# Optimization experiments

Hardware: AMD Instinct MI355X
Metric: run time of the kernel (lower is better)

The kernel has to match this reference:

```python
import jax, jax.numpy as jnp
from jax import lax
import numpy as np

GAMMA, WARP = 0.01, 134.4          # SoftDTW(gamma=0.01, warp=134.4)
INF, BIG = 100000.0, 1e9           # INF from kl_loss_sdtw; BIG ~ math.inf boundary
KL_A, KL_FWD_A, GEN_A, GEN_E2E_A, FEAT_A, DUR_A, MEL_A = 1.0, 1.0, 1.0, 1.0, 1.0, 1.0, 45.0


def soft_dtw(D):
    """Soft-DTW with warp penalty. D: [B, N, M] -> R[:, N, M].
    R[i,j] = D[i-1,j-1] + softmin_gamma(R[i-1,j-1], R[i-1,j]+warp, R[i,j-1]+warp)."""
    B, N, M = D.shape
    row0 = jnp.full((B, M + 1), BIG, D.dtype).at[:, 0].set(0.0)  # R[0, :]

    def row_step(prev_row, d_row):                 # prev_row: [B, M+1], d_row: [B, M]
        left0 = jnp.full((B,), BIG, D.dtype)       # R[i, 0]

        def col_step(r_left, inp):
            d, r_diag, r_up = inp                  # each [B]
            r0 = -r_diag / GAMMA
            r1 = -(r_up + WARP) / GAMMA
            r2 = -(r_left + WARP) / GAMMA
            rmax = jnp.maximum(jnp.maximum(r0, r1), r2)
            smin = -GAMMA * (jnp.log(jnp.exp(r0 - rmax) + jnp.exp(r1 - rmax) + jnp.exp(r2 - rmax)) + rmax)
            r = d + smin
            return r, r

        xs = (d_row.T, prev_row[:, :-1].T, prev_row[:, 1:].T)   # scan over j=1..M
        _, vals = lax.scan(col_step, left0, xs)                 # [M, B]
        new_row = jnp.concatenate([left0[:, None], vals.T], axis=1)
        return new_row, None

    last, _ = lax.scan(row_step, row0, jnp.swapaxes(D, 0, 1))   # scan over i=1..N
    return last[:, M]


def sdtw_kl_matrix(z, logs_q, m, logs_p):
    """kl[b,i,j] = sum_h logs_p - logs_q - 0.5 + 0.5*(z-m)^2*exp(-2 logs_p).
    m, logs_p: [b,h,tp]; z, logs_q: [b,h,tq] -> [b,tp,tq] via 3 batched GEMMs."""
    h = m.shape[1]
    w = jnp.exp(-2.0 * logs_p)                                   # [b,h,tp]
    quad = (jnp.einsum('bhi,bhj->bij', w, z * z)
            - 2.0 * jnp.einsum('bhi,bhj->bij', w * m, z)
            + jnp.sum(w * m * m, axis=1)[:, :, None])
    return (jnp.sum(logs_p, axis=1)[:, :, None]
            - jnp.sum(logs_q, axis=1)[:, None, :]
            - 0.5 * h + 0.5 * quad)


def kl_loss_sdtw(z, logs_q, m, logs_p, p_mask, q_mask):
    kl = sdtw_kl_matrix(z, logs_q, m, logs_p)
    kl = jnp.pad(kl, ((0, 0), (0, 1), (0, 1)))
    pm = jnp.pad(p_mask, ((0, 0), (0, 1)))
    qm = jnp.pad(q_mask, ((0, 0), (0, 1)))
    pb = pm[:, :, None].astype(bool)
    qb = qm[:, None, :].astype(bool)
    kl = jnp.where(pb ^ qb, INF, kl)
    kl = jnp.where((~pb) & (~qb), 0.0, kl)
    return jnp.sum(soft_dtw(kl)) / jnp.sum(pm)


def _forward(mel_slice, mel_slice_hat, scores_disc_fake, scores_disc_fake_e2e,
             feats_disc_real, feats_disc_fake, loss_duration, loss_duration_len,
             loss_pitch, z_p, m_p, logs_p, z_q, m_q, logs_q, p_mask, z_mask):
    # generator losses: sum over discriminators of mean((1-score)^2)
    loss_gen = jnp.sum(jnp.mean((1.0 - scores_disc_fake) ** 2, axis=(1, 2))) * GEN_A
    loss_gen_e2e = jnp.sum(jnp.mean((1.0 - scores_disc_fake_e2e) ** 2, axis=(1, 2))) * GEN_E2E_A
    # feature-matching loss (real feats detached)
    fr = lax.stop_gradient(feats_disc_real)
    loss_fm = jnp.sum(jnp.mean(jnp.abs(fr - feats_disc_fake), axis=(1, 2, 3))) * 2.0 * FEAT_A
    loss_mel = jnp.mean(jnp.abs(mel_slice - mel_slice_hat)) * MEL_A
    loss_dur = jnp.sum(loss_duration) * DUR_A
    loss_dur_len = jnp.log(loss_duration_len + 1e-6)
    zm = z_mask[:, 0, :]
    loss_kl = kl_loss_sdtw(z_p, logs_q, m_p, logs_p, p_mask, zm) * KL_A
    loss_kl_fwd = kl_loss_sdtw(z_q, logs_p, m_q, logs_q, zm, p_mask) * KL_FWD_A
    return (loss_gen + loss_gen_e2e + loss_fm + loss_mel + loss_dur
            + loss_dur_len + loss_kl + loss_kl_fwd)


def setup_inputs() -> dict:
    key = jax.random.key(0)
    ks = jax.random.split(key, 16)
    B, H, TP, TQ = 4, 192, 350, 400
    return {
        'mel_slice': jax.random.normal(ks[0], (B, 80, 128), jnp.float32),
        'mel_slice_hat': jax.random.normal(ks[1], (B, 80, 128), jnp.float32),
        'scores_disc_fake': jax.random.normal(ks[2], (6, B, 8192), jnp.float32),
        'scores_disc_fake_e2e': jax.random.normal(ks[3], (6, B, 8192), jnp.float32),
        'feats_disc_real': jax.random.normal(ks[4], (24, B, 128, 4096), jnp.float32),
        'feats_disc_fake': jax.random.normal(ks[5], (24, B, 128, 4096), jnp.float32),
        'loss_duration': jax.random.uniform(ks[6], (B, TP), jnp.float32) * 0.01,
        'loss_duration_len': jax.random.uniform(ks[7], (), jnp.float32) + 0.5,
        'loss_pitch': jax.random.uniform(ks[8], (B, TP), jnp.float32),
        'z_p': jax.random.normal(ks[9], (B, H, TQ), jnp.float32),
        'm_p': jax.random.normal(ks[10], (B, H, TP), jnp.float32),
        'logs_p': 0.1 * jax.random.normal(ks[11], (B, H, TP), jnp.float32),
        'z_q': jax.random.normal(ks[12], (B, H, TP), jnp.float32),
        'm_q': jax.random.normal(ks[13], (B, H, TQ), jnp.float32),
        'logs_q': 0.1 * jax.random.normal(ks[14], (B, H, TQ), jnp.float32),
        'p_mask': jnp.ones((B, TP), jnp.float32),
        'z_mask': jnp.ones((B, 1, TQ), jnp.float32),
    }


def reference(mel_slice, mel_slice_hat, scores_disc_fake, scores_disc_fake_e2e,
              feats_disc_real, feats_disc_fake, loss_duration, loss_duration_len,
              loss_pitch, z_p, m_p, logs_p, z_q, m_q, logs_q, p_mask, z_mask):
    return _forward(mel_slice, mel_slice_hat, scores_disc_fake, scores_disc_fake_e2e,
                    feats_disc_real, feats_disc_fake, loss_duration, loss_duration_len,
                    loss_pitch, z_p, m_p, logs_p, z_q, m_q, logs_q, p_mask, z_mask)
```

## Files before the change

kernel.cpp:

```cpp
#include <hip/hip_runtime.h>
#include <math.h>

#define GAMMA_ 0.01f
#define WARP_  134.4f
#define INFV   100000.0f
#define BIGV   1000000000.0f

#define B_  4
#define H_  192
#define TP_ 350
#define TQ_ 400

#define ACC_OFF 0
#define DTW_OFF 16
#define SLP_OFF 32
#define SLQ_OFF (SLP_OFF + B_*TP_)
#define KL1_OFF 3072
#define KL1_NCOL 401
#define KL1_PITCHT 352
#define KL2_OFF (KL1_OFF + B_*KL1_NCOL*KL1_PITCHT)
#define KL2_NCOL 351
#define KL2_PITCHT 408

#define RING_SLOTS 67
#define RING_PITCH 416

typedef float f4_t __attribute__((ext_vector_type(4)));

__device__ __forceinline__ unsigned pk2(float a, float b) {
    unsigned ua = __float_as_uint(a), ub = __float_as_uint(b);
    ua = (ua + 0x7FFFu + ((ua >> 16) & 1u)) >> 16;
    ub = (ub + 0x7FFFu + ((ub >> 16) & 1u)) & 0xFFFF0000u;
    return ua | ub;
}
__device__ __forceinline__ int modS(int x) { return x - (x / RING_SLOTS) * RING_SLOTS; }

__global__ void sl_kernel(const float* __restrict__ logs_p,
                          const float* __restrict__ logs_q,
                          float* __restrict__ ws) {
    int t = blockIdx.x * 256 + threadIdx.x;
    if (t < 32) ws[ACC_OFF + t] = 0.f;
    if (t < B_ * TP_) {
        int b = t / TP_, i = t % TP_;
        const float* p = logs_p + (size_t)b * H_ * TP_ + i;
        float s = 0.f;
        for (int h = 0; h < H_; ++h) s += p[(size_t)h * TP_];
        ws[SLP_OFF + t] = s;
    } else if (t < B_ * TP_ + B_ * TQ_) {
        int t2 = t - B_ * TP_;
        int b = t2 / TQ_, j = t2 % TQ_;
        const float* p = logs_q + (size_t)b * H_ * TQ_ + j;
        float s = 0.f;
        for (int h = 0; h < H_; ++h) s += p[(size_t)h * TQ_];
        ws[SLQ_OFF + t2] = s;
    }
}

__global__ void kl_kernel(const float* __restrict__ mp, const float* __restrict__ lsp,
                          const float* __restrict__ zp,
                          const float* __restrict__ mq, const float* __restrict__ lsq,
                          const float* __restrict__ zq,
                          const float* __restrict__ pmask, const float* __restrict__ zmask,
                          float* __restrict__ ws) {
    int which = blockIdx.z >> 2;
    int b     = blockIdx.z & 3;
    const float *mS, *lS, *zS, *SLrow, *SLcol, *rm, *cm; float* out; int R, C, pitchT;
    if (which == 0) { mS=mp; lS=lsp; zS=zp; SLrow=ws+SLP_OFF; SLcol=ws+SLQ_OFF;
                      rm=pmask + b*TP_; cm=zmask + b*TQ_;
                      out=ws+KL1_OFF + (size_t)b*KL1_NCOL*KL1_PITCHT;
                      R=TP_; C=TQ_; pitchT=KL1_PITCHT; }
    else            { mS=mq; lS=lsq; zS=zq; SLrow=ws+SLQ_OFF; SLcol=ws+SLP_OFF;
                      rm=zmask + b*TQ_; cm=pmask + b*TP_;
                      out=ws+KL2_OFF + (size_t)b*KL2_NCOL*KL2_PITCHT;
                      R=TQ_; C=TP_; pitchT=KL2_PITCHT; }
// ... 23 lines not shown
            zSh[hh][cc] = (gj < C) ? zB[(size_t)h * C + gj] : 0.f;
        }
        __syncthreads();
#pragma unroll
        for (int kk = 0; kk < 16; ++kk) {
            float2 wv = *(const float2*)&wS [kk][tx * 2];
            float2 mv = *(const float2*)&mSh[kk][tx * 2];
            float2 zv = *(const float2*)&zSh[kk][ty * 2];
            float d;
            d = zv.x - mv.x; a00 += wv.x * d * d;
            d = zv.x - mv.y; a01 += wv.y * d * d;
            d = zv.y - mv.x; a10 += wv.x * d * d;
            d = zv.y - mv.y; a11 += wv.y * d * d;
        }
        __syncthreads();
    }
    float accs[2][2] = {{a00, a01}, {a10, a11}};
    for (int jj = 0; jj < 2; ++jj)
        for (int ii = 0; ii < 2; ++ii) {
            int I = i0 + tx * 2 + ii, J = j0 + ty * 2 + jj;
            if (I <= R && J <= C) {
                bool pbI = (I < R) && (rm[I] != 0.f);
                bool qbJ = (J < C) && (cm[J] != 0.f);
                float v;
                if (pbI & qbJ)
                    v = SLrow[b * R + I] - SLcol[b * C + J] - 0.5f * H_ + 0.5f * accs[jj][ii];
                else
                    v = (pbI ^ qbJ) ? INFV : 0.f;
                out[(size_t)J * pitchT + I] = v;
            }
        }
}

#define SLD2(BK, q) { int col_; \
    col_ = ((q) << 3) + cA; \
    if (vA && col_ <= C_) rA##BK = *(const f4_t*)(klT + (size_t)col_ * pitchT + (iA << 2)); \
    col_ = ((q) << 3) + cB; \
    if (vB && col_ <= C_) rB##BK = *(const f4_t*)(klT + (size_t)col_ * pitchT + (iB << 2)); }
#define SST2(BK, q) { int col_; \
    col_ = ((q) << 3) + cA; \
    if (vA && col_ <= C_) { int s_ = modS(col_); \
        uint2 u_; u_.x = pk2(rA##BK.x, rA##BK.y); u_.y = pk2(rA##BK.z, rA##BK.w); \
        *(uint2*)&ring[s_][iA << 2] = u_; } \
    col_ = ((q) << 3) + cB; \
    if (vB && col_ <= C_) { int s_ = modS(col_); \
        uint2 u_; u_.x = pk2(rB##BK.x, rB##BK.y); u_.y = pk2(rB##BK.z, rB##BK.w); \
        *(uint2*)&ring[s_][iB << 2] = u_; } }

#define STAGER_BAR() { asm volatile("s_waitcnt lgkmcnt(0)" ::: "memory"); \
                       __builtin_amdgcn_s_barrier(); }

__global__ __launch_bounds__(512, 1) void main_kernel(
    const float* __restrict__ mel, const float* __restrict__ melh,
    const float* __restrict__ sg,  const float* __restrict__ se,
    const float* __restrict__ fr,  const float* __restrict__ ff,
    const float* __restrict__ dur, float* ws) {
    __shared__ __align__(16) unsigned short ring[RING_SLOTS + 2][RING_PITCH];
    int bid = blockIdx.x, tid = threadIdx.x;
    if (bid < 8) {
        int b = bid & 3, which = bid >> 2;
        int R_, C_, pitchT;
        const float* klT;
        if (which == 0) {
            R_ = TP_; C_ = TQ_; pitchT = KL1_PITCHT;
            klT = ws + KL1_OFF + (size_t)b * KL1_NCOL * KL1_PITCHT;
        } else {
            R_ = TQ_; C_ = TP_; pitchT = KL2_PITCHT;
            klT = ws + KL2_OFF + (size_t)b * KL2_NCOL * KL2_PITCHT;
        }
        int lres = R_ >> 3;
        int kres = R_ & 7;
        int tmax = C_ + lres;
        int P = (tmax >> 3) + 1;

        if (tid < 64) {
            int lane = tid; bool lane0 = (lane == 0);
            float p0=BIGV,p1=BIGV,p2=BIGV,p3=BIGV,p4=BIGV,p5=BIGV,p6=BIGV,p7=BIGV;
            float recv_cur = BIGV, recv_prev = BIGV;
            __syncthreads();
            for (int ph = 0; ph < P; ++ph) {
                int t0 = ph << 3;
                int c0 = t0 - lane;
                int cr = c0 < 0 ? 0 : (c0 > C_ ? C_ : c0);
                int s0 = modS(cr);
                int4 rd = *(const int4*)&ring[s0][lane << 3];
#pragma unroll
                for (int i = 0; i < 8; ++i) {
                    int c = t0 + i - lane;
                    int4 ru = rd;
                    if (i < 7) {
                        int cn = c + 1; cn = cn < 0 ? 0 : (cn > C_ ? C_ : cn);
                        int sn = modS(cn);
                        rd = *(const int4*)&ring[sn][lane << 3];
                    }
                    float last_ = 0.f;
                    if ((unsigned)c <= (unsigned)C_) {
                        float u_  = lane0 ? BIGV : recv_cur;
                        float dg  = (c == 0) ? (lane0 ? 0.f : BIGV) : (lane0 ? BIGV : recv_prev);
                        float d0 = __uint_as_float((unsigned)ru.x << 16);
                        float d1 = __uint_as_float((unsigned)ru.x & 0xFFFF0000u);
                        float d2 = __uint_as_float((unsigned)ru.y << 16);
                        float d3 = __uint_as_float((unsigned)ru.y & 0xFFFF0000u);
                        float d4 = __uint_as_float((unsigned)ru.z << 16);
                        float d5 = __uint_as_float((unsigned)ru.z & 0xFFFF0000u);
                        float d6 = __uint_as_float((unsigned)ru.w << 16);
                        float d7 = __uint_as_float((unsigned)ru.w & 0xFFFF0000u);
                        float B0 = WARP_ + d0, B1 = WARP_ + d1, B2 = WARP_ + d2, B3 = WARP_ + d3;
                        float B4 = WARP_ + d4, B5 = WARP_ + d5, B6 = WARP_ + d6, B7 = WARP_ + d7;
                        float P0 = fminf(dg + d0, p0 + B0);
                        float P1 = fminf(p0 + d1, p1 + B1);
                        float P2 = fminf(p1 + d2, p2 + B2);
                        float P3 = fminf(p2 + d3, p3 + B3);
                        float P4 = fminf(p3 + d4, p4 + B4);
                        float P5 = fminf(p4 + d5, p5 + B5);
                        float P6 = fminf(p5 + d6, p6 + B6);
                        float P7 = fminf(p6 + d7, p7 + B7);
                        u_ = fminf(P0, u_ + B0); p0 = u_;
                        u_ = fminf(P1, u_ + B1); p1 = u_;
                        u_ = fminf(P2, u_ + B2); p2 = u_;
                        u_ = fminf(P3, u_ + B3); p3 = u_;
                        u_ = fminf(P4, u_ + B4); p4 = u_;
                        u_ = fminf(P5, u_ + B5); p5 = u_;
                        u_ = fminf(P6, u_ + B6); p6 = u_;
                        u_ = fminf(P7, u_ + B7); p7 = u_;
                        last_ = u_;
                    }
                    recv_prev = recv_cur;
                    recv_cur  = __shfl_up(last_, 1);
                }
                __syncthreads();
            }
            float q0 = __shfl(p0, lres), q1 = __shfl(p1, lres), q2 = __shfl(p2, lres),
                  q3 = __shfl(p3, lres), q4 = __shfl(p4, lres), q5 = __shfl(p5, lres),
                  q6 = __shfl(p6, lres), q7 = __shfl(p7, lres);
            if (lane0) {
                float res = (kres == 0) ? q0 : (kres == 1) ? q1 : (kres == 2) ? q2 :
                            (kres == 3) ? q3 : (kres == 4) ? q4 : (kres == 5) ? q5 :
                            (kres == 6) ? q6 : q7;
                ws[DTW_OFF + which * 4 + b] = res;
            }
        } else {
            int st  = tid - 64;
            int n4  = pitchT >> 2;
            int tot = n4 << 3;
            int cA = st / n4,  iA = st - cA * n4;
            int eB = st + 448; int cB = eB / n4, iB = eB - cB * n4;
            bool vA = st < tot, vB = eB < tot;
            f4_t rA0={0,0,0,0}, rA1={0,0,0,0}, rA2={0,0,0,0}, rA3={0,0,0,0};
            f4_t rB0={0,0,0,0}, rB1={0,0,0,0}, rB2={0,0,0,0}, rB3={0,0,0,0};
            SLD2(0, 0)
            SST2(0, 0)
            SLD2(1, 1)
            STAGER_BAR();
            for (int p = 0; p < P; ++p) {
                switch ((p + 1) & 3) {
                    case 0: SST2(0, p + 1) break;
                    case 1: SST2(1, p + 1) break;
                    case 2: SST2(2, p + 1) break;
                    default: SST2(3, p + 1) break;
                }
                if ((p & 3) == 0) {
                    SLD2(2, p + 2) SLD2(3, p + 3) SLD2(0, p + 4) SLD2(1, p + 5)
                }
                STAGER_BAR();
            }
        }
    } else {
        int rid = bid - 8;
        long T = (long)(gridDim.x - 8) * 512;
        long gid = (long)rid * 512 + tid;
        const float4* fr4   = (const float4*)fr;
        const float4* ff4   = (const float4*)ff;
        const float4* sg4   = (const float4*)sg;
        const float4* se4   = (const float4*)se;
        const float4* mel4  = (const float4*)mel;
        const float4* melh4 = (const float4*)melh;
        const float4* dur4  = (const float4*)dur;
        const long E0 = 12582912;
        float a2 = 0.f;
        long v = gid;
        for (; v + T < E0; v += 2 * T) {
            float4 x0 = fr4[v],     y0 = ff4[v];
            float4 x1 = fr4[v + T], y1 = ff4[v + T];
            a2 += fabsf(x0.x-y0.x)+fabsf(x0.y-y0.y)+fabsf(x0.z-y0.z)+fabsf(x0.w-y0.w);
            a2 += fabsf(x1.x-y1.x)+fabsf(x1.y-y1.y)+fabsf(x1.z-y1.z)+fabsf(x1.w-y1.w);
        }
        for (; v < E0; v += T) {
            float4 x = fr4[v], y = ff4[v];
            a2 += fabsf(x.x-y.x)+fabsf(x.y-y.y)+fabsf(x.z-y.z)+fabsf(x.w-y.w);
        }
        float a0=0.f, a1=0.f, a3=0.f, a4=0.f;
        long w = gid;
        if (w < 108894) {
            if (w < 49152) {
                float4 s = sg4[w]; float e;
                e=1.f-s.x; a0+=e*e; e=1.f-s.y; a0+=e*e; e=1.f-s.z; a0+=e*e; e=1.f-s.w; a0+=e*e;
            } else if (w < 98304) {
                float4 s = se4[w - 49152]; float e;
                e=1.f-s.x; a1+=e*e; e=1.f-s.y; a1+=e*e; e=1.f-s.z; a1+=e*e; e=1.f-s.w; a1+=e*e;
            } else if (w < 108544) {
                float4 x = mel4[w - 98304], y = melh4[w - 98304];
                a3 += fabsf(x.x-y.x)+fabsf(x.y-y.y)+fabsf(x.z-y.z)+fabsf(x.w-y.w);
            } else {
                float4 x = dur4[w - 108544]; a4 += x.x + x.y + x.z + x.w;
            }
        }
        float vals[5] = {a0, a1, a2, a3, a4};
        float* sb = (float*)ring;
#pragma unroll
        for (int q = 0; q < 5; ++q) {
            float x = vals[q];
            for (int off = 32; off > 0; off >>= 1) x += __shfl_xor(x, off);
            if ((tid & 63) == 0) sb[(tid >> 6) * 8 + q] = x;
        }
        __syncthreads();
        if (tid < 5) {
            float s = 0.f;
            for (int w2 = 0; w2 < 8; ++w2) s += sb[w2 * 8 + tid];
            atomicAdd(&ws[ACC_OFF + tid], s);
        }
    }
}

__global__ void masksum_kernel(const float* __restrict__ pmask,
                               const float* __restrict__ zmask,
                               float* __restrict__ ws) {
    int tid = threadIdx.x;
    float a5 = 0.f, a6 = 0.f;
    for (int v = tid; v < B_ * TP_; v += 256) a5 += pmask[v];
    for (int v = tid; v < B_ * TQ_; v += 256) a6 += zmask[v];
    __shared__ float s5[4], s6[4];
    for (int off = 32; off > 0; off >>= 1) { a5 += __shfl_xor(a5, off); a6 += __shfl_xor(a6, off); }
    if ((tid & 63) == 0) { s5[tid >> 6] = a5; s6[tid >> 6] = a6; }
    __syncthreads();
    if (tid == 0) {
        ws[5] = s5[0] + s5[1] + s5[2] + s5[3];
        ws[6] = s6[0] + s6[1] + s6[2] + s6[3];
    }
}

__global__ void final_kernel(const float* __restrict__ ws,
                             const float* __restrict__ ldl,
                             float* __restrict__ out) {
    if (threadIdx.x == 0 && blockIdx.x == 0) {
        float gen  = ws[0] * (1.f / 32768.f);
        float e2e  = ws[1] * (1.f / 32768.f);
        float fm   = ws[2] * (2.f / 2097152.f);
        float melv = ws[3] * (45.f / 40960.f);
        float durv = ws[4];
        float dlen = logf(ldl[0] + 1e-6f);
        float kl  = (ws[DTW_OFF + 0] + ws[DTW_OFF + 1] + ws[DTW_OFF + 2] + ws[DTW_OFF + 3]) / ws[5];
        float klf = (ws[DTW_OFF + 4] + ws[DTW_OFF + 5] + ws[DTW_OFF + 6] + ws[DTW_OFF + 7]) / ws[6];
        out[0] = gen + e2e + fm + melv + durv + dlen + kl + klf;
    }
}

extern "C" void kernel_launch(void* const* d_in, const int* in_sizes, int n_in,
                              void* d_out, int out_size, void* d_ws, size_t ws_size,
                              hipStream_t stream) {
    const float* mel    = (const float*)d_in[0];
    const float* melh   = (const float*)d_in[1];
    const float* sg     = (const float*)d_in[2];
    const float* se     = (const float*)d_in[3];
    const float* fr     = (const float*)d_in[4];
    const float* ff     = (const float*)d_in[5];
    const float* dur    = (const float*)d_in[6];
    const float* ldl    = (const float*)d_in[7];
    const float* z_p    = (const float*)d_in[9];
    const float* m_p    = (const float*)d_in[10];
    const float* logs_p = (const float*)d_in[11];
    const float* z_q    = (const float*)d_in[12];
    const float* m_q    = (const float*)d_in[13];
    const float* logs_q = (const float*)d_in[14];
    const float* pmask  = (const float*)d_in[15];
    const float* zmask  = (const float*)d_in[16];
    float* ws  = (float*)d_ws;
    float* out = (float*)d_out;

    sl_kernel<<<12, 256, 0, stream>>>(logs_p, logs_q, ws);
    masksum_kernel<<<1, 256, 0, stream>>>(pmask, zmask, ws);
    kl_kernel<<<dim3(13, 13, 8), dim3(16, 16), 0, stream>>>(
        m_p, logs_p, z_p, m_q, logs_q, z_q, pmask, zmask, ws);
    main_kernel<<<8 + 1016, 512, 0, stream>>>(mel, melh, sg, se, fr, ff, dur, ws);
    final_kernel<<<1, 64, 0, stream>>>(ws, ldl, out);
}
```

Before: 200.5 us.

## Split DTW and reductions into separate kernels, fold masksum into sl_kernel

Splits the fused main kernel into a dedicated 8-block DTW kernel and a separate 1016-block reduction kernel launched one after the other on the same stream. The mask-sum kernel is folded into sl_kernel as an extra block, and the zeroing of the accumulators skips the two slots that block writes. The DTW stager drops its 4-deep register prefetch with a raw s_barrier for a single-buffer load/store with __syncthreads. The split removes the overlap between the serial DTW and the bandwidth-bound reductions, so their times now add. The simpler stager also hides less global-load latency.

```diff
diff --git a/kernel.cpp b/kernel.cpp
--- a/kernel.cpp
+++ b/kernel.cpp
@@ -37,9 +37,26 @@
 
 __global__ void sl_kernel(const float* __restrict__ logs_p,
                           const float* __restrict__ logs_q,
+                          const float* __restrict__ pmask,
+                          const float* __restrict__ zmask,
                           float* __restrict__ ws) {
+    if (blockIdx.x == 12) {
+        int tid = threadIdx.x;
+        float a5 = 0.f, a6 = 0.f;
+        for (int v = tid; v < B_ * TP_; v += 256) a5 += pmask[v];
+        for (int v = tid; v < B_ * TQ_; v += 256) a6 += zmask[v];
+        __shared__ float s5[4], s6[4];
+        for (int off = 32; off > 0; off >>= 1) { a5 += __shfl_xor(a5, off); a6 += __shfl_xor(a6, off); }
+        if ((tid & 63) == 0) { s5[tid >> 6] = a5; s6[tid >> 6] = a6; }
+        __syncthreads();
+        if (tid == 0) {
+            ws[5] = s5[0] + s5[1] + s5[2] + s5[3];
+            ws[6] = s6[0] + s6[1] + s6[2] + s6[3];
+        }
+        return;
+    }
     int t = blockIdx.x * 256 + threadIdx.x;
-    if (t < 32) ws[ACC_OFF + t] = 0.f;
+    if (t < 32 && t != 5 && t != 6) ws[ACC_OFF + t] = 0.f;
     if (t < B_ * TP_) {
         int b = t / TP_, i = t % TP_;
         const float* p = logs_p + (size_t)b * H_ * TP_ + i;
@@ -129,210 +146,174 @@
         }
 }
 
-#define SLD2(BK, q) { int col_; \
-    col_ = ((q) << 3) + cA; \
-    if (vA && col_ <= C_) rA##BK = *(const f4_t*)(klT + (size_t)col_ * pitchT + (iA << 2)); \
-    col_ = ((q) << 3) + cB; \
-    if (vB && col_ <= C_) rB##BK = *(const f4_t*)(klT + (size_t)col_ * pitchT + (iB << 2)); }
-#define SST2(BK, q) { int col_; \
-    col_ = ((q) << 3) + cA; \
-    if (vA && col_ <= C_) { int s_ = modS(col_); \
-        uint2 u_; u_.x = pk2(rA##BK.x, rA##BK.y); u_.y = pk2(rA##BK.z, rA##BK.w); \
-        *(uint2*)&ring[s_][iA << 2] = u_; } \
-    col_ = ((q) << 3) + cB; \
-    if (vB && col_ <= C_) { int s_ = modS(col_); \
-        uint2 u_; u_.x = pk2(rB##BK.x, rB##BK.y); u_.y = pk2(rB##BK.z, rB##BK.w); \
-        *(uint2*)&ring[s_][iB << 2] = u_; } }
-
-#define STAGER_BAR() { asm volatile("s_waitcnt lgkmcnt(0)" ::: "memory"); \
-                       __builtin_amdgcn_s_barrier(); }
-
-__global__ __launch_bounds__(512, 1) void main_kernel(
+#define SLD(q, r, cc, ii, vv) { int col_ = ((q) << 3) + (cc); \
+    if ((vv) && col_ <= C_) r = *(const f4_t*)(klT + (size_t)col_ * pitchT + ((ii) << 2)); }
+#define SST(q, r, cc, ii, vv) { int col_ = ((q) << 3) + (cc); \
+    if ((vv) && col_ <= C_) { int s_ = modS(col_); \
+        uint2 u_; u_.x = pk2(r.x, r.y); u_.y = pk2(r.z, r.w); \
+        *(uint2*)&ring[s_][(ii) << 2] = u_; } }
+
+__global__ __launch_bounds__(512, 1) void dtw_kernel(float* ws) {
+    __shared__ __align__(16) unsigned short ring[RING_SLOTS + 2][RING_PITCH];
+    int bid = blockIdx.x, tid = threadIdx.x;
+    int b = bid & 3, which = bid >> 2;
+    int R_, C_, pitchT;
+    const float* klT;
+    if (which == 0) {
+        R_ = TP_; C_ = TQ_; pitchT = KL1_PITCHT;
+        klT = ws + KL1_OFF + (size_t)b * KL1_NCOL * KL1_PITCHT;
+    } else {
+        R_ = TQ_; C_ = TP_; pitchT = KL2_PITCHT;
+        klT = ws + KL2_OFF + (size_t)b * KL2_NCOL * KL2_PITCHT;
+    }
+    int lres = R_ >> 3;
+    int kres = R_ & 7;
+    int tmax = C_ + lres;
+    int P = (tmax >> 3) + 1;
+
+    if (tid < 64) {
+        int lane = tid; bool lane0 = (lane == 0);
+        float p0=BIGV,p1=BIGV,p2=BIGV,p3=BIGV,p4=BIGV,p5=BIGV,p6=BIGV,p7=BIGV;
+        float recv_cur = BIGV, recv_prev = BIGV;
+        __syncthreads();
+        for (int ph = 0; ph < P; ++ph) {
+            int t0 = ph << 3;
+            int c0 = t0 - lane;
+            int cr = c0 < 0 ? 0 : (c0 > C_ ? C_ : c0);
+            int s0 = modS(cr);
+            int4 rd = *(const int4*)&ring[s0][lane << 3];
+#pragma unroll
+            for (int i = 0; i < 8; ++i) {
+                int c = t0 + i - lane;
+                int4 ru = rd;
+                if (i < 7) {
+                    int cn = c + 1; cn = cn < 0 ? 0 : (cn > C_ ? C_ : cn);
+                    int sn = modS(cn);
+                    rd = *(const int4*)&ring[sn][lane << 3];
+                }
+                float last_ = 0.f;
+                if ((unsigned)c <= (unsigned)C_) {
+                    float u_  = lane0 ? BIGV : recv_cur;
+                    float dg  = (c == 0) ? (lane0 ? 0.f : BIGV) : (lane0 ? BIGV : recv_prev);
+                    float d0 = __uint_as_float((unsigned)ru.x << 16);
+                    float d1 = __uint_as_float((unsigned)ru.x & 0xFFFF0000u);
+                    float d2 = __uint_as_float((unsigned)ru.y << 16);
+                    float d3 = __uint_as_float((unsigned)ru.y & 0xFFFF0000u);
+                    float d4 = __uint_as_float((unsigned)ru.z << 16);
+                    float d5 = __uint_as_float((unsigned)ru.z & 0xFFFF0000u);
+                    float d6 = __uint_as_float((unsigned)ru.w << 16);
+                    float d7 = __uint_as_float((unsigned)ru.w & 0xFFFF0000u);
+                    float B0 = WARP_ + d0, B1 = WARP_ + d1, B2 = WARP_ + d2, B3 = WARP_ + d3;
+                    float B4 = WARP_ + d4, B5 = WARP_ + d5, B6 = WARP_ + d6, B7 = WARP_ + d7;
+                    float P0 = fminf(dg + d0, p0 + B0);
+                    float P1 = fminf(p0 + d1, p1 + B1);
+                    float P2 = fminf(p1 + d2, p2 + B2);
+                    float P3 = fminf(p2 + d3, p3 + B3);
+                    float P4 = fminf(p3 + d4, p4 + B4);
+                    float P5 = fminf(p4 + d5, p5 + B5);
+                    float P6 = fminf(p5 + d6, p6 + B6);
+                    float P7 = fminf(p6 + d7, p7 + B7);
+                    u_ = fminf(P0, u_ + B0); p0 = u_;
+                    u_ = fminf(P1, u_ + B1); p1 = u_;
+                    u_ = fminf(P2, u_ + B2); p2 = u_;
+                    u_ = fminf(P3, u_ + B3); p3 = u_;
+                    u_ = fminf(P4, u_ + B4); p4 = u_;
+                    u_ = fminf(P5, u_ + B5); p5 = u_;
+                    u_ = fminf(P6, u_ + B6); p6 = u_;
+                    u_ = fminf(P7, u_ + B7); p7 = u_;
+                    last_ = u_;
+                }
+                recv_prev = recv_cur;
+                recv_cur  = __shfl_up(last_, 1);
+            }
+            __syncthreads();
+        }
+        float q0 = __shfl(p0, lres), q1 = __shfl(p1, lres), q2 = __shfl(p2, lres),
+              q3 = __shfl(p3, lres), q4 = __shfl(p4, lres), q5 = __shfl(p5, lres),
+              q6 = __shfl(p6, lres), q7 = __shfl(p7, lres);
+        if (lane0) {
+            float res = (kres == 0) ? q0 : (kres == 1) ? q1 : (kres == 2) ? q2 :
+                        (kres == 3) ? q3 : (kres == 4) ? q4 : (kres == 5) ? q5 :
+                        (kres == 6) ? q6 : q7;
+            ws[DTW_OFF + which * 4 + b] = res;
+        }
+    } else {
+        int st  = tid - 64;
+        int n4  = pitchT >> 2;
+        int tot = n4 << 3;
+        int cA = st / n4,  iA = st - cA * n4;
+        int eB = st + 448; int cB = eB / n4, iB = eB - cB * n4;
+        bool vA = st < tot, vB = eB < tot;
+        f4_t rA = {0.f,0.f,0.f,0.f}, rB = {0.f,0.f,0.f,0.f};
+        SLD(0, rA, cA, iA, vA) SLD(0, rB, cB, iB, vB)
+        SST(0, rA, cA, iA, vA) SST(0, rB, cB, iB, vB)
+        SLD(1, rA, cA, iA, vA) SLD(1, rB, cB, iB, vB)
+        __syncthreads();
+        for (int p = 0; p < P; ++p) {
+            SST(p + 1, rA, cA, iA, vA) SST(p + 1, rB, cB, iB, vB)
+            SLD(p + 2, rA, cA, iA, vA) SLD(p + 2, rB, cB, iB, vB)
+            __syncthreads();
+        }
+    }
+}
+
+__global__ __launch_bounds__(512) void red_kernel(
     const float* __restrict__ mel, const float* __restrict__ melh,
     const float* __restrict__ sg,  const float* __restrict__ se,
     const float* __restrict__ fr,  const float* __restrict__ ff,
     const float* __restrict__ dur, float* ws) {
-    __shared__ __align__(16) unsigned short ring[RING_SLOTS + 2][RING_PITCH];
-    int bid = blockIdx.x, tid = threadIdx.x;
-    if (bid < 8) {
-        int b = bid & 3, which = bid >> 2;
-        int R_, C_, pitchT;
-        const float* klT;
-        if (which == 0) {
-            R_ = TP_; C_ = TQ_; pitchT = KL1_PITCHT;
-            klT = ws + KL1_OFF + (size_t)b * KL1_NCOL * KL1_PITCHT;
+    __shared__ float sb[64];
+    int tid = threadIdx.x;
+    long T = (long)gridDim.x * 512;
+    long gid = (long)blockIdx.x * 512 + tid;
+    const float4* fr4   = (const float4*)fr;
+    const float4* ff4   = (const float4*)ff;
+    const float4* sg4   = (const float4*)sg;
+    const float4* se4   = (const float4*)se;
+    const float4* mel4  = (const float4*)mel;
+    const float4* melh4 = (const float4*)melh;
+    const float4* dur4  = (const float4*)dur;
+    const long E0 = 12582912;
+    float a2 = 0.f;
+    long v = gid;
+    for (; v + T < E0; v += 2 * T) {
+        float4 x0 = fr4[v],     y0 = ff4[v];
+        float4 x1 = fr4[v + T], y1 = ff4[v + T];
+        a2 += fabsf(x0.x-y0.x)+fabsf(x0.y-y0.y)+fabsf(x0.z-y0.z)+fabsf(x0.w-y0.w);
+        a2 += fabsf(x1.x-y1.x)+fabsf(x1.y-y1.y)+fabsf(x1.z-y1.z)+fabsf(x1.w-y1.w);
+    }
+    for (; v < E0; v += T) {
+        float4 x = fr4[v], y = ff4[v];
+        a2 += fabsf(x.x-y.x)+fabsf(x.y-y.y)+fabsf(x.z-y.z)+fabsf(x.w-y.w);
+    }
+    float a0=0.f, a1=0.f, a3=0.f, a4=0.f;
+    long w = gid;
+    if (w < 108894) {
+        if (w < 49152) {
+            float4 s = sg4[w]; float e;
+            e=1.f-s.x; a0+=e*e; e=1.f-s.y; a0+=e*e; e=1.f-s.z; a0+=e*e; e=1.f-s.w; a0+=e*e;
+        } else if (w < 98304) {
+            float4 s = se4[w - 49152]; float e;
+            e=1.f-s.x; a1+=e*e; e=1.f-s.y; a1+=e*e; e=1.f-s.z; a1+=e*e; e=1.f-s.w; a1+=e*e;
+        } else if (w < 108544) {
+            float4 x = mel4[w - 98304], y = melh4[w - 98304];
+            a3 += fabsf(x.x-y.x)+fabsf(x.y-y.y)+fabsf(x.z-y.z)+fabsf(x.w-y.w);
         } else {
-            R_ = TQ_; C_ = TP_; pitchT = KL2_PITCHT;
-            klT = ws + KL2_OFF + (size_t)b * KL2_NCOL * KL2_PITCHT;
-        }
-        int lres = R_ >> 3;
-        int kres = R_ & 7;
-        int tmax = C_ + lres;
-        int P = (tmax >> 3) + 1;
-
-        if (tid < 64) {
-            int lane = tid; bool lane0 = (lane == 0);
-            float p0=BIGV,p1=BIGV,p2=BIGV,p3=BIGV,p4=BIGV,p5=BIGV,p6=BIGV,p7=BIGV;
-            float recv_cur = BIGV, recv_prev = BIGV;
-            __syncthreads();
-            for (int ph = 0; ph < P; ++ph) {
-                int t0 = ph << 3;
-                int c0 = t0 - lane;
-                int cr = c0 < 0 ? 0 : (c0 > C_ ? C_ : c0);
-                int s0 = modS(cr);
-                int4 rd = *(const int4*)&ring[s0][lane << 3];
+            float4 x = dur4[w - 108544]; a4 += x.x + x.y + x.z + x.w;
+        }
+    }
+    float vals[5] = {a0, a1, a2, a3, a4};
 #pragma unroll
-                for (int i = 0; i < 8; ++i) {
-                    int c = t0 + i - lane;
-                    int4 ru = rd;
-                    if (i < 7) {
-                        int cn = c + 1; cn = cn < 0 ? 0 : (cn > C_ ? C_ : cn);
-                        int sn = modS(cn);
-                        rd = *(const int4*)&ring[sn][lane << 3];
-                    }
-                    float last_ = 0.f;
-                    if ((unsigned)c <= (unsigned)C_) {
-                        float u_  = lane0 ? BIGV : recv_cur;
-                        float dg  = (c == 0) ? (lane0 ? 0.f : BIGV) : (lane0 ? BIGV : recv_prev);
-                        float d0 = __uint_as_float((unsigned)ru.x << 16);
-                        float d1 = __uint_as_float((unsigned)ru.x & 0xFFFF0000u);
-                        float d2 = __uint_as_float((unsigned)ru.y << 16);
-                        float d3 = __uint_as_float((unsigned)ru.y & 0xFFFF0000u);
-                        float d4 = __uint_as_float((unsigned)ru.z << 16);
-                        float d5 = __uint_as_float((unsigned)ru.z & 0xFFFF0000u);
-                        float d6 = __uint_as_float((unsigned)ru.w << 16);
-                        float d7 = __uint_as_float((unsigned)ru.w & 0xFFFF0000u);
-                        float B0 = WARP_ + d0, B1 = WARP_ + d1, B2 = WARP_ + d2, B3 = WARP_ + d3;
-                        float B4 = WARP_ + d4, B5 = WARP_ + d5, B6 = WARP_ + d6, B7 = WARP_ + d7;
-                        float P0 = fminf(dg + d0, p0 + B0);
-                        float P1 = fminf(p0 + d1, p1 + B1);
-                        float P2 = fminf(p1 + d2, p2 + B2);
-                        float P3 = fminf(p2 + d3, p3 + B3);
-                        float P4 = fminf(p3 + d4, p4 + B4);
-                        float P5 = fminf(p4 + d5, p5 + B5);
-                        float P6 = fminf(p5 + d6, p6 + B6);
-                        float P7 = fminf(p6 + d7, p7 + B7);
-                        u_ = fminf(P0, u_ + B0); p0 = u_;
-                        u_ = fminf(P1, u_ + B1); p1 = u_;
-                        u_ = fminf(P2, u_ + B2); p2 = u_;
-                        u_ = fminf(P3, u_ + B3); p3 = u_;
-                        u_ = fminf(P4, u_ + B4); p4 = u_;
-                        u_ = fminf(P5, u_ + B5); p5 = u_;
-                        u_ = fminf(P6, u_ + B6); p6 = u_;
-                        u_ = fminf(P7, u_ + B7); p7 = u_;
-                        last_ = u_;
-                    }
-                    recv_prev = recv_cur;
-                    recv_cur  = __shfl_up(last_, 1);
-                }
-                __syncthreads();
-            }
-            float q0 = __shfl(p0, lres), q1 = __shfl(p1, lres), q2 = __shfl(p2, lres),
-                  q3 = __shfl(p3, lres), q4 = __shfl(p4, lres), q5 = __shfl(p5, lres),
-                  q6 = __shfl(p6, lres), q7 = __shfl(p7, lres);
-            if (lane0) {
-                float res = (kres == 0) ? q0 : (kres == 1) ? q1 : (kres == 2) ? q2 :
-                            (kres == 3) ? q3 : (kres == 4) ? q4 : (kres == 5) ? q5 :
-                            (kres == 6) ? q6 : q7;
-                ws[DTW_OFF + which * 4 + b] = res;
-            }
-        } else {
-            int st  = tid - 64;
-            int n4  = pitchT >> 2;
-            int tot = n4 << 3;
-            int cA = st / n4,  iA = st - cA * n4;
-            int eB = st + 448; int cB = eB / n4, iB = eB - cB * n4;
-            bool vA = st < tot, vB = eB < tot;
-            f4_t rA0={0,0,0,0}, rA1={0,0,0,0}, rA2={0,0,0,0}, rA3={0,0,0,0};
-            f4_t rB0={0,0,0,0}, rB1={0,0,0,0}, rB2={0,0,0,0}, rB3={0,0,0,0};
-            SLD2(0, 0)
-            SST2(0, 0)
-            SLD2(1, 1)
-            STAGER_BAR();
-            for (int p = 0; p < P; ++p) {
-                switch ((p + 1) & 3) {
-                    case 0: SST2(0, p + 1) break;
-                    case 1: SST2(1, p + 1) break;
-                    case 2: SST2(2, p + 1) break;
-                    default: SST2(3, p + 1) break;
-                }
-                if ((p & 3) == 0) {
-                    SLD2(2, p + 2) SLD2(3, p + 3) SLD2(0, p + 4) SLD2(1, p + 5)
-                }
-                STAGER_BAR();
-            }
-        }
-    } else {
-        int rid = bid - 8;
-        long T = (long)(gridDim.x - 8) * 512;
-        long gid = (long)rid * 512 + tid;
-        const float4* fr4   = (const float4*)fr;
-        const float4* ff4   = (const float4*)ff;
-        const float4* sg4   = (const float4*)sg;
-        const float4* se4   = (const float4*)se;
-        const float4* mel4  = (const float4*)mel;
-        const float4* melh4 = (const float4*)melh;
-        const float4* dur4  = (const float4*)dur;
-        const long E0 = 12582912;
-        float a2 = 0.f;
-        long v = gid;
-        for (; v + T < E0; v += 2 * T) {
-            float4 x0 = fr4[v],     y0 = ff4[v];
-            float4 x1 = fr4[v + T], y1 = ff4[v + T];
-            a2 += fabsf(x0.x-y0.x)+fabsf(x0.y-y0.y)+fabsf(x0.z-y0.z)+fabsf(x0.w-y0.w);
-            a2 += fabsf(x1.x-y1.x)+fabsf(x1.y-y1.y)+fabsf(x1.z-y1.z)+fabsf(x1.w-y1.w);
-        }
-        for (; v < E0; v += T) {
-            float4 x = fr4[v], y = ff4[v];
-            a2 += fabsf(x.x-y.x)+fabsf(x.y-y.y)+fabsf(x.z-y.z)+fabsf(x.w-y.w);
-        }
-        float a0=0.f, a1=0.f, a3=0.f, a4=0.f;
-        long w = gid;
-        if (w < 108894) {
-            if (w < 49152) {
-                float4 s = sg4[w]; float e;
-                e=1.f-s.x; a0+=e*e; e=1.f-s.y; a0+=e*e; e=1.f-s.z; a0+=e*e; e=1.f-s.w; a0+=e*e;
-            } else if (w < 98304) {
-                float4 s = se4[w - 49152]; float e;
-                e=1.f-s.x; a1+=e*e; e=1.f-s.y; a1+=e*e; e=1.f-s.z; a1+=e*e; e=1.f-s.w; a1+=e*e;
-            } else if (w < 108544) {
-                float4 x = mel4[w - 98304], y = melh4[w - 98304];
-                a3 += fabsf(x.x-y.x)+fabsf(x.y-y.y)+fabsf(x.z-y.z)+fabsf(x.w-y.w);
-            } else {
-                float4 x = dur4[w - 108544]; a4 += x.x + x.y + x.z + x.w;
-            }
-        }
-        float vals[5] = {a0, a1, a2, a3, a4};
-        float* sb = (float*)ring;
-#pragma unroll
-        for (int q = 0; q < 5; ++q) {
-            float x = vals[q];
-            for (int off = 32; off > 0; off >>= 1) x += __shfl_xor(x, off);
-            if ((tid & 63) == 0) sb[(tid >> 6) * 8 + q] = x;
-        }
-        __syncthreads();
-        if (tid < 5) {
-            float s = 0.f;
-            for (int w2 = 0; w2 < 8; ++w2) s += sb[w2 * 8 + tid];
-            atomicAdd(&ws[ACC_OFF + tid], s);
-        }
-    }
-}
-
-__global__ void masksum_kernel(const float* __restrict__ pmask,
-                               const float* __restrict__ zmask,
-                               float* __restrict__ ws) {
-    int tid = threadIdx.x;
-    float a5 = 0.f, a6 = 0.f;
-    for (int v = tid; v < B_ * TP_; v += 256) a5 += pmask[v];
-    for (int v = tid; v < B_ * TQ_; v += 256) a6 += zmask[v];
-    __shared__ float s5[4], s6[4];
-    for (int off = 32; off > 0; off >>= 1) { a5 += __shfl_xor(a5, off); a6 += __shfl_xor(a6, off); }
-    if ((tid & 63) == 0) { s5[tid >> 6] = a5; s6[tid >> 6] = a6; }
+    for (int q = 0; q < 5; ++q) {
+        float x = vals[q];
+        for (int off = 32; off > 0; off >>= 1) x += __shfl_xor(x, off);
+        if ((tid & 63) == 0) sb[(tid >> 6) * 8 + q] = x;
+    }
     __syncthreads();
-    if (tid == 0) {
-        ws[5] = s5[0] + s5[1] + s5[2] + s5[3];
-        ws[6] = s6[0] + s6[1] + s6[2] + s6[3];
+    if (tid < 5) {
+        float s = 0.f;
+        for (int w2 = 0; w2 < 8; ++w2) s += sb[w2 * 8 + tid];
+        atomicAdd(&ws[ACC_OFF + tid], s);
     }
 }
 
@@ -374,10 +355,10 @@
     float* ws  = (float*)d_ws;
     float* out = (float*)d_out;
 
-    sl_kernel<<<12, 256, 0, stream>>>(logs_p, logs_q, ws);
-    masksum_kernel<<<1, 256, 0, stream>>>(pmask, zmask, ws);
+    sl_kernel<<<13, 256, 0, stream>>>(logs_p, logs_q, pmask, zmask, ws);
     kl_kernel<<<dim3(13, 13, 8), dim3(16, 16), 0, stream>>>(
         m_p, logs_p, z_p, m_q, logs_q, z_q, pmask, zmask, ws);
-    main_kernel<<<8 + 1016, 512, 0, stream>>>(mel, melh, sg, se, fr, ff, dur, ws);
+    dtw_kernel<<<8, 512, 0, stream>>>(ws);
+    red_kernel<<<1016, 512, 0, stream>>>(mel, melh, sg, se, fr, ff, dur, ws);
     final_kernel<<<1, 64, 0, stream>>>(ws, ldl, out);
 }
```

Result: slower. 206.6 us (+3.1%).

## Split DTW and reduction into separate kernels, fold mask sums into sl_kernel

Applied to the files above, without the earlier changes.

The combined main kernel is split into an 8-block dtw_kernel and a separate red_kernel. red_kernel no longer reserves the large LDS ring buffer and has no occupancy hint of one block per CU, so more reduction blocks can be resident at once. It also launches more blocks (2040), unrolls the feature-map L1 loop four times and uses nontemporal loads. The mask-sum launch is folded into an extra block of sl_kernel to save one kernel launch. The trade-off is that the latency-bound DTW recurrence and the bandwidth-bound reductions now run one after the other on the same stream instead of overlapping.

```diff
diff --git a/kernel.cpp b/kernel.cpp
--- a/kernel.cpp
+++ b/kernel.cpp
@@ -37,9 +37,26 @@
 
 __global__ void sl_kernel(const float* __restrict__ logs_p,
                           const float* __restrict__ logs_q,
+                          const float* __restrict__ pmask,
+                          const float* __restrict__ zmask,
                           float* __restrict__ ws) {
+    if (blockIdx.x == 12) {
+        int tid = threadIdx.x;
+        float a5 = 0.f, a6 = 0.f;
+        for (int v = tid; v < B_ * TP_; v += 256) a5 += pmask[v];
+        for (int v = tid; v < B_ * TQ_; v += 256) a6 += zmask[v];
+        __shared__ float s5[4], s6[4];
+        for (int off = 32; off > 0; off >>= 1) { a5 += __shfl_xor(a5, off); a6 += __shfl_xor(a6, off); }
+        if ((tid & 63) == 0) { s5[tid >> 6] = a5; s6[tid >> 6] = a6; }
+        __syncthreads();
+        if (tid == 0) {
+            ws[5] = s5[0] + s5[1] + s5[2] + s5[3];
+            ws[6] = s6[0] + s6[1] + s6[2] + s6[3];
+        }
+        return;
+    }
     int t = blockIdx.x * 256 + threadIdx.x;
-    if (t < 32) ws[ACC_OFF + t] = 0.f;
+    if (t < 32 && t != 5 && t != 6) ws[ACC_OFF + t] = 0.f;
     if (t < B_ * TP_) {
         int b = t / TP_, i = t % TP_;
         const float* p = logs_p + (size_t)b * H_ * TP_ + i;
@@ -147,192 +164,184 @@
 #define STAGER_BAR() { asm volatile("s_waitcnt lgkmcnt(0)" ::: "memory"); \
                        __builtin_amdgcn_s_barrier(); }
 
-__global__ __launch_bounds__(512, 1) void main_kernel(
+__global__ __launch_bounds__(512, 1) void dtw_kernel(float* ws) {
+    __shared__ __align__(16) unsigned short ring[RING_SLOTS + 2][RING_PITCH];
+    int bid = blockIdx.x, tid = threadIdx.x;
+    int b = bid & 3, which = bid >> 2;
+    int R_, C_, pitchT;
+    const float* klT;
+    if (which == 0) {
+        R_ = TP_; C_ = TQ_; pitchT = KL1_PITCHT;
+        klT = ws + KL1_OFF + (size_t)b * KL1_NCOL * KL1_PITCHT;
+    } else {
+        R_ = TQ_; C_ = TP_; pitchT = KL2_PITCHT;
+        klT = ws + KL2_OFF + (size_t)b * KL2_NCOL * KL2_PITCHT;
+    }
+    int lres = R_ >> 3;
+    int kres = R_ & 7;
+    int tmax = C_ + lres;
+    int P = (tmax >> 3) + 1;
+
+    if (tid < 64) {
+        int lane = tid; bool lane0 = (lane == 0);
+        float p0=BIGV,p1=BIGV,p2=BIGV,p3=BIGV,p4=BIGV,p5=BIGV,p6=BIGV,p7=BIGV;
+        float recv_cur = BIGV, recv_prev = BIGV;
+        __syncthreads();
+        for (int ph = 0; ph < P; ++ph) {
+            int t0 = ph << 3;
+            int c0 = t0 - lane;
+            int cr = c0 < 0 ? 0 : (c0 > C_ ? C_ : c0);
+            int s0 = modS(cr);
+            int4 rd = *(const int4*)&ring[s0][lane << 3];
+#pragma unroll
+            for (int i = 0; i < 8; ++i) {
+                int c = t0 + i - lane;
+                int4 ru = rd;
+                if (i < 7) {
+                    int cn = c + 1; cn = cn < 0 ? 0 : (cn > C_ ? C_ : cn);
+                    int sn = modS(cn);
+                    rd = *(const int4*)&ring[sn][lane << 3];
+                }
+                float last_ = 0.f;
+                if ((unsigned)c <= (unsigned)C_) {
+                    float u_  = lane0 ? BIGV : recv_cur;
+                    float dg  = (c == 0) ? (lane0 ? 0.f : BIGV) : (lane0 ? BIGV : recv_prev);
+                    float d0 = __uint_as_float((unsigned)ru.x << 16);
+                    float d1 = __uint_as_float((unsigned)ru.x & 0xFFFF0000u);
+                    float d2 = __uint_as_float((unsigned)ru.y << 16);
+                    float d3 = __uint_as_float((unsigned)ru.y & 0xFFFF0000u);
+                    float d4 = __uint_as_float((unsigned)ru.z << 16);
+                    float d5 = __uint_as_float((unsigned)ru.z & 0xFFFF0000u);
+                    float d6 = __uint_as_float((unsigned)ru.w << 16);
+                    float d7 = __uint_as_float((unsigned)ru.w & 0xFFFF0000u);
+                    float B0 = WARP_ + d0, B1 = WARP_ + d1, B2 = WARP_ + d2, B3 = WARP_ + d3;
+                    float B4 = WARP_ + d4, B5 = WARP_ + d5, B6 = WARP_ + d6, B7 = WARP_ + d7;
+                    float P0 = fminf(dg + d0, p0 + B0);
+                    float P1 = fminf(p0 + d1, p1 + B1);
+                    float P2 = fminf(p1 + d2, p2 + B2);
+                    float P3 = fminf(p2 + d3, p3 + B3);
+                    float P4 = fminf(p3 + d4, p4 + B4);
+                    float P5 = fminf(p4 + d5, p5 + B5);
+                    float P6 = fminf(p5 + d6, p6 + B6);
+                    float P7 = fminf(p6 + d7, p7 + B7);
+                    u_ = fminf(P0, u_ + B0); p0 = u_;
+                    u_ = fminf(P1, u_ + B1); p1 = u_;
+                    u_ = fminf(P2, u_ + B2); p2 = u_;
+                    u_ = fminf(P3, u_ + B3); p3 = u_;
+                    u_ = fminf(P4, u_ + B4); p4 = u_;
+                    u_ = fminf(P5, u_ + B5); p5 = u_;
+                    u_ = fminf(P6, u_ + B6); p6 = u_;
+                    u_ = fminf(P7, u_ + B7); p7 = u_;
+                    last_ = u_;
+                }
+                recv_prev = recv_cur;
+                recv_cur  = __shfl_up(last_, 1);
+            }
+            __syncthreads();
+        }
+        float q0 = __shfl(p0, lres), q1 = __shfl(p1, lres), q2 = __shfl(p2, lres),
+              q3 = __shfl(p3, lres), q4 = __shfl(p4, lres), q5 = __shfl(p5, lres),
+              q6 = __shfl(p6, lres), q7 = __shfl(p7, lres);
+        if (lane0) {
+            float res = (kres == 0) ? q0 : (kres == 1) ? q1 : (kres == 2) ? q2 :
+                        (kres == 3) ? q3 : (kres == 4) ? q4 : (kres == 5) ? q5 :
+                        (kres == 6) ? q6 : q7;
+            ws[DTW_OFF + which * 4 + b] = res;
+        }
+    } else {
+        int st  = tid - 64;
+        int n4  = pitchT >> 2;
+        int tot = n4 << 3;
+        int cA = st / n4,  iA = st - cA * n4;
+        int eB = st + 448; int cB = eB / n4, iB = eB - cB * n4;
+        bool vA = st < tot, vB = eB < tot;
+        f4_t rA0={0,0,0,0}, rA1={0,0,0,0}, rA2={0,0,0,0}, rA3={0,0,0,0};
+        f4_t rB0={0,0,0,0}, rB1={0,0,0,0}, rB2={0,0,0,0}, rB3={0,0,0,0};
+        SLD2(0, 0)
+        SST2(0, 0)
+        SLD2(1, 1)
+        STAGER_BAR();
+        for (int p = 0; p < P; ++p) {
+            switch ((p + 1) & 3) {
+                case 0: SST2(0, p + 1) break;
+                case 1: SST2(1, p + 1) break;
+                case 2: SST2(2, p + 1) break;
+                default: SST2(3, p + 1) break;
+            }
+            if ((p & 3) == 0) {
+                SLD2(2, p + 2) SLD2(3, p + 3) SLD2(0, p + 4) SLD2(1, p + 5)
+            }
+            STAGER_BAR();
+        }
+    }
+}
+
+__global__ __launch_bounds__(512) void red_kernel(
     const float* __restrict__ mel, const float* __restrict__ melh,
     const float* __restrict__ sg,  const float* __restrict__ se,
     const float* __restrict__ fr,  const float* __restrict__ ff,
     const float* __restrict__ dur, float* ws) {
-    __shared__ __align__(16) unsigned short ring[RING_SLOTS + 2][RING_PITCH];
-    int bid = blockIdx.x, tid = threadIdx.x;
-    if (bid < 8) {
-        int b = bid & 3, which = bid >> 2;
-        int R_, C_, pitchT;
-        const float* klT;
-        if (which == 0) {
-            R_ = TP_; C_ = TQ_; pitchT = KL1_PITCHT;
-            klT = ws + KL1_OFF + (size_t)b * KL1_NCOL * KL1_PITCHT;
+    __shared__ float sb[64];
+    int tid = threadIdx.x;
+    long T = (long)gridDim.x * 512;
+    long gid = (long)blockIdx.x * 512 + tid;
+    const f4_t* fr4   = (const f4_t*)fr;
+    const f4_t* ff4   = (const f4_t*)ff;
+    const float4* sg4   = (const float4*)sg;
+    const float4* se4   = (const float4*)se;
+    const float4* mel4  = (const float4*)mel;
+    const float4* melh4 = (const float4*)melh;
+    const float4* dur4  = (const float4*)dur;
+    const long E0 = 12582912;
+    float a2 = 0.f;
+    long v = gid;
+    for (; v + 3 * T < E0; v += 4 * T) {
+        f4_t x0 = __builtin_nontemporal_load(fr4 + v);
+        f4_t y0 = __builtin_nontemporal_load(ff4 + v);
+        f4_t x1 = __builtin_nontemporal_load(fr4 + v + T);
+        f4_t y1 = __builtin_nontemporal_load(ff4 + v + T);
+        f4_t x2 = __builtin_nontemporal_load(fr4 + v + 2 * T);
+        f4_t y2 = __builtin_nontemporal_load(ff4 + v + 2 * T);
+        f4_t x3 = __builtin_nontemporal_load(fr4 + v + 3 * T);
+        f4_t y3 = __builtin_nontemporal_load(ff4 + v + 3 * T);
+        a2 += fabsf(x0.x-y0.x)+fabsf(x0.y-y0.y)+fabsf(x0.z-y0.z)+fabsf(x0.w-y0.w);
+        a2 += fabsf(x1.x-y1.x)+fabsf(x1.y-y1.y)+fabsf(x1.z-y1.z)+fabsf(x1.w-y1.w);
+        a2 += fabsf(x2.x-y2.x)+fabsf(x2.y-y2.y)+fabsf(x2.z-y2.z)+fabsf(x2.w-y2.w);
+        a2 += fabsf(x3.x-y3.x)+fabsf(x3.y-y3.y)+fabsf(x3.z-y3.z)+fabsf(x3.w-y3.w);
+    }
+    for (; v < E0; v += T) {
+        f4_t x = __builtin_nontemporal_load(fr4 + v);
+        f4_t y = __builtin_nontemporal_load(ff4 + v);
+        a2 += fabsf(x.x-y.x)+fabsf(x.y-y.y)+fabsf(x.z-y.z)+fabsf(x.w-y.w);
+    }
+    float a0=0.f, a1=0.f, a3=0.f, a4=0.f;
+    long w = gid;
+    if (w < 108894) {
+        if (w < 49152) {
+            float4 s = sg4[w]; float e;
+            e=1.f-s.x; a0+=e*e; e=1.f-s.y; a0+=e*e; e=1.f-s.z; a0+=e*e; e=1.f-s.w; a0+=e*e;
+        } else if (w < 98304) {
+            float4 s = se4[w - 49152]; float e;
+            e=1.f-s.x; a1+=e*e; e=1.f-s.y; a1+=e*e; e=1.f-s.z; a1+=e*e; e=1.f-s.w; a1+=e*e;
+        } else if (w < 108544) {
+            float4 x = mel4[w - 98304], y = melh4[w - 98304];
+            a3 += fabsf(x.x-y.x)+fabsf(x.y-y.y)+fabsf(x.z-y.z)+fabsf(x.w-y.w);
         } else {
-            R_ = TQ_; C_ = TP_; pitchT = KL2_PITCHT;
-            klT = ws + KL2_OFF + (size_t)b * KL2_NCOL * KL2_PITCHT;
-        }
-        int lres = R_ >> 3;
-        int kres = R_ & 7;
-        int tmax = C_ + lres;
-        int P = (tmax >> 3) + 1;
-
-        if (tid < 64) {
-            int lane = tid; bool lane0 = (lane == 0);
-            float p0=BIGV,p1=BIGV,p2=BIGV,p3=BIGV,p4=BIGV,p5=BIGV,p6=BIGV,p7=BIGV;
-            float recv_cur = BIGV, recv_prev = BIGV;
-            __syncthreads();
-            for (int ph = 0; ph < P; ++ph) {
-                int t0 = ph << 3;
-                int c0 = t0 - lane;
-                int cr = c0 < 0 ? 0 : (c0 > C_ ? C_ : c0);
-                int s0 = modS(cr);
-                int4 rd = *(const int4*)&ring[s0][lane << 3];
+            float4 x = dur4[w - 108544]; a4 += x.x + x.y + x.z + x.w;
+        }
+    }
+    float vals[5] = {a0, a1, a2, a3, a4};
 #pragma unroll
-                for (int i = 0; i < 8; ++i) {
-                    int c = t0 + i - lane;
-                    int4 ru = rd;
-                    if (i < 7) {
-                        int cn = c + 1; cn = cn < 0 ? 0 : (cn > C_ ? C_ : cn);
-                        int sn = modS(cn);
-                        rd = *(const int4*)&ring[sn][lane << 3];
-                    }
-                    float last_ = 0.f;
-                    if ((unsigned)c <= (unsigned)C_) {
-                        float u_  = lane0 ? BIGV : recv_cur;
-                        float dg  = (c == 0) ? (lane0 ? 0.f : BIGV) : (lane0 ? BIGV : recv_prev);
-                        float d0 = __uint_as_float((unsigned)ru.x << 16);
-                        float d1 = __uint_as_float((unsigned)ru.x & 0xFFFF0000u);
-                        float d2 = __uint_as_float((unsigned)ru.y << 16);
-                        float d3 = __uint_as_float((unsigned)ru.y & 0xFFFF0000u);
-                        float d4 = __uint_as_float((unsigned)ru.z << 16);
-                        float d5 = __uint_as_float((unsigned)ru.z & 0xFFFF0000u);
-                        float d6 = __uint_as_float((unsigned)ru.w << 16);
-                        float d7 = __uint_as_float((unsigned)ru.w & 0xFFFF0000u);
-                        float B0 = WARP_ + d0, B1 = WARP_ + d1, B2 = WARP_ + d2, B3 = WARP_ + d3;
-                        float B4 = WARP_ + d4, B5 = WARP_ + d5, B6 = WARP_ + d6, B7 = WARP_ + d7;
-                        float P0 = fminf(dg + d0, p0 + B0);
-                        float P1 = fminf(p0 + d1, p1 + B1);
-                        float P2 = fminf(p1 + d2, p2 + B2);
-                        float P3 = fminf(p2 + d3, p3 + B3);
-                        float P4 = fminf(p3 + d4, p4 + B4);
-                        float P5 = fminf(p4 + d5, p5 + B5);
-                        float P6 = fminf(p5 + d6, p6 + B6);
-                        float P7 = fminf(p6 + d7, p7 + B7);
-                        u_ = fminf(P0, u_ + B0); p0 = u_;
-                        u_ = fminf(P1, u_ + B1); p1 = u_;
-                        u_ = fminf(P2, u_ + B2); p2 = u_;
-                        u_ = fminf(P3, u_ + B3); p3 = u_;
-                        u_ = fminf(P4, u_ + B4); p4 = u_;
-                        u_ = fminf(P5, u_ + B5); p5 = u_;
-                        u_ = fminf(P6, u_ + B6); p6 = u_;
-                        u_ = fminf(P7, u_ + B7); p7 = u_;
-                        last_ = u_;
-                    }
-                    recv_prev = recv_cur;
-                    recv_cur  = __shfl_up(last_, 1);
-                }
-                __syncthreads();
-            }
-            float q0 = __shfl(p0, lres), q1 = __shfl(p1, lres), q2 = __shfl(p2, lres),
-                  q3 = __shfl(p3, lres), q4 = __shfl(p4, lres), q5 = __shfl(p5, lres),
-                  q6 = __shfl(p6, lres), q7 = __shfl(p7, lres);
-            if (lane0) {
-                float res = (kres == 0) ? q0 : (kres == 1) ? q1 : (kres == 2) ? q2 :
-                            (kres == 3) ? q3 : (kres == 4) ? q4 : (kres == 5) ? q5 :
-                            (kres == 6) ? q6 : q7;
-                ws[DTW_OFF + which * 4 + b] = res;
-            }
-        } else {
-            int st  = tid - 64;
-            int n4  = pitchT >> 2;
-            int tot = n4 << 3;
-            int cA = st / n4,  iA = st - cA * n4;
-            int eB = st + 448; int cB = eB / n4, iB = eB - cB * n4;
-            bool vA = st < tot, vB = eB < tot;
-            f4_t rA0={0,0,0,0}, rA1={0,0,0,0}, rA2={0,0,0,0}, rA3={0,0,0,0};
-            f4_t rB0={0,0,0,0}, rB1={0,0,0,0}, rB2={0,0,0,0}, rB3={0,0,0,0};
-            SLD2(0, 0)
-            SST2(0, 0)
-            SLD2(1, 1)
-            STAGER_BAR();
-            for (int p = 0; p < P; ++p) {
-                switch ((p + 1) & 3) {
-                    case 0: SST2(0, p + 1) break;
-                    case 1: SST2(1, p + 1) break;
-                    case 2: SST2(2, p + 1) break;
-                    default: SST2(3, p + 1) break;
-                }
-                if ((p & 3) == 0) {
-                    SLD2(2, p + 2) SLD2(3, p + 3) SLD2(0, p + 4) SLD2(1, p + 5)
-                }
-                STAGER_BAR();
-            }
-        }
-    } else {
-        int rid = bid - 8;
-        long T = (long)(gridDim.x - 8) * 512;
-        long gid = (long)rid * 512 + tid;
-        const float4* fr4   = (const float4*)fr;
-        const float4* ff4   = (const float4*)ff;
-        const float4* sg4   = (const float4*)sg;
-        const float4* se4   = (const float4*)se;
-        const float4* mel4  = (const float4*)mel;
-        const float4* melh4 = (const float4*)melh;
-        const float4* dur4  = (const float4*)dur;
-        const long E0 = 12582912;
-        float a2 = 0.f;
-        long v = gid;
-        for (; v + T < E0; v += 2 * T) {
-            float4 x0 = fr4[v],     y0 = ff4[v];
-            float4 x1 = fr4[v + T], y1 = ff4[v + T];
-            a2 += fabsf(x0.x-y0.x)+fabsf(x0.y-y0.y)+fabsf(x0.z-y0.z)+fabsf(x0.w-y0.w);
-            a2 += fabsf(x1.x-y1.x)+fabsf(x1.y-y1.y)+fabsf(x1.z-y1.z)+fabsf(x1.w-y1.w);
-        }
-        for (; v < E0; v += T) {
-            float4 x = fr4[v], y = ff4[v];
-            a2 += fabsf(x.x-y.x)+fabsf(x.y-y.y)+fabsf(x.z-y.z)+fabsf(x.w-y.w);
-        }
-        float a0=0.f, a1=0.f, a3=0.f, a4=0.f;
-        long w = gid;
-        if (w < 108894) {
-            if (w < 49152) {
-                float4 s = sg4[w]; float e;
-                e=1.f-s.x; a0+=e*e; e=1.f-s.y; a0+=e*e; e=1.f-s.z; a0+=e*e; e=1.f-s.w; a0+=e*e;
-            } else if (w < 98304) {
-                float4 s = se4[w - 49152]; float e;
-                e=1.f-s.x; a1+=e*e; e=1.f-s.y; a1+=e*e; e=1.f-s.z; a1+=e*e; e=1.f-s.w; a1+=e*e;
-            } else if (w < 108544) {
-                float4 x = mel4[w - 98304], y = melh4[w - 98304];
-                a3 += fabsf(x.x-y.x)+fabsf(x.y-y.y)+fabsf(x.z-y.z)+fabsf(x.w-y.w);
-            } else {
-                float4 x = dur4[w - 108544]; a4 += x.x + x.y + x.z + x.w;
-            }
-        }
-        float vals[5] = {a0, a1, a2, a3, a4};
-        float* sb = (float*)ring;
-#pragma unroll
-        for (int q = 0; q < 5; ++q) {
-            float x = vals[q];
-            for (int off = 32; off > 0; off >>= 1) x += __shfl_xor(x, off);
-            if ((tid & 63) == 0) sb[(tid >> 6) * 8 + q] = x;
-        }
-        __syncthreads();
-        if (tid < 5) {
-            float s = 0.f;
-            for (int w2 = 0; w2 < 8; ++w2) s += sb[w2 * 8 + tid];
-            atomicAdd(&ws[ACC_OFF + tid], s);
-        }
-    }
-}
-
-__global__ void masksum_kernel(const float* __restrict__ pmask,
-                               const float* __restrict__ zmask,
-                               float* __restrict__ ws) {
-    int tid = threadIdx.x;
-    float a5 = 0.f, a6 = 0.f;
-    for (int v = tid; v < B_ * TP_; v += 256) a5 += pmask[v];
-    for (int v = tid; v < B_ * TQ_; v += 256) a6 += zmask[v];
-    __shared__ float s5[4], s6[4];
-    for (int off = 32; off > 0; off >>= 1) { a5 += __shfl_xor(a5, off); a6 += __shfl_xor(a6, off); }
-    if ((tid & 63) == 0) { s5[tid >> 6] = a5; s6[tid >> 6] = a6; }
+    for (int q = 0; q < 5; ++q) {
+        float x = vals[q];
+        for (int off = 32; off > 0; off >>= 1) x += __shfl_xor(x, off);
+        if ((tid & 63) == 0) sb[(tid >> 6) * 8 + q] = x;
+    }
     __syncthreads();
-    if (tid == 0) {
-        ws[5] = s5[0] + s5[1] + s5[2] + s5[3];
-        ws[6] = s6[0] + s6[1] + s6[2] + s6[3];
+    if (tid < 5) {
+        float s = 0.f;
+        for (int w2 = 0; w2 < 8; ++w2) s += sb[w2 * 8 + tid];
+        atomicAdd(&ws[ACC_OFF + tid], s);
     }
 }
 
@@ -374,10 +383,10 @@
     float* ws  = (float*)d_ws;
     float* out = (float*)d_out;
 
-    sl_kernel<<<12, 256, 0, stream>>>(logs_p, logs_q, ws);
-    masksum_kernel<<<1, 256, 0, stream>>>(pmask, zmask, ws);
+    sl_kernel<<<13, 256, 0, stream>>>(logs_p, logs_q, pmask, zmask, ws);
     kl_kernel<<<dim3(13, 13, 8), dim3(16, 16), 0, stream>>>(
         m_p, logs_p, z_p, m_q, logs_q, z_q, pmask, zmask, ws);
-    main_kernel<<<8 + 1016, 512, 0, stream>>>(mel, melh, sg, se, fr, ff, dur, ws);
+    dtw_kernel<<<8, 512, 0, stream>>>(ws);
+    red_kernel<<<2040, 512, 0, stream>>>(mel, melh, sg, se, fr, ff, dur, ws);
     final_kernel<<<1, 64, 0, stream>>>(ws, ldl, out);
 }
```

Measured after the change: 214.8 us. 7.2% more time.
